# Kernel tuning notes

Hardware: AMD Instinct MI355X
Metric: run time of the kernel (lower is better)

The kernel has to match this reference:

```python
import jax, jax.numpy as jnp
import numpy as np

NH, HD = 12, 64          # heads, head dim (d_model=768)
SC = HD ** -0.5          # both Attention and CA_Attention use head_dim**-0.5


def patchify(x, p1, p2):
    # 'b c (h p1) (w p2) -> b (h w) (p1 p2 c)'
    B, C, H, W = x.shape
    h, w = H // p1, W // p2
    x = x.reshape(B, C, h, p1, w, p2).transpose(0, 2, 4, 3, 5, 1)  # b h w p1 p2 c
    return x.reshape(B, h * w, p1 * p2 * C)


def unpatchify(x, h, w, p1, p2, c):
    # 'b (h w) (p1 p2 c) -> b c (h p1) (w p2)'
    B = x.shape[0]
    x = x.reshape(B, h, w, p1, p2, c).transpose(0, 5, 1, 3, 2, 4)
    return x.reshape(B, c, h * p1, w * p2)


def ln(x, g, b):
    m = x.mean(-1, keepdims=True)
    v = ((x - m) ** 2).mean(-1, keepdims=True)
    return (x - m) / jnp.sqrt(v + 1e-5) * g + b


def setup_inputs() -> dict:
    key = jax.random.key(0)
    specs = [
        ('img_feats', (2, 32, 112, 112, 80)), ('txt', (2, 77, 768)),
        ('pe_w_ax', (1120, 768)), ('pe_b_ax', (768,)),
        ('pe_w_sag', (1120, 768)), ('pe_b_sag', (768,)),
        ('pe_w_cor', (1568, 768)), ('pe_b_cor', (768,)),
        ('pos_ax', (1, 256, 768)), ('pos_sag', (1, 256, 768)), ('pos_cor', (1, 256, 768)),
        ('qw', (768, 768)), ('kw', (768, 768)), ('vw', (768, 768)),
        ('pw', (768, 768)), ('pb', (768,)),
        ('caq_w', (768, 768)), ('caq_b', (768,)), ('cak_w', (768, 768)), ('cak_b', (768,)),
        ('cav_w', (768, 768)), ('cav_b', (768,)), ('cao_w', (768, 768)), ('cao_b', (768,)),
        ('mlp_w1', (768, 3072)), ('mlp_b1', (3072,)), ('mlp_w2', (3072, 768)), ('mlp_b2', (768,)),
        ('ow_ax', (768, 1120)), ('ob_ax', (1120,)),
        ('ow_sag', (768, 1120)), ('ob_sag', (1120,)),
        ('ow_cor', (768, 1568)), ('ob_cor', (1568,)),
    ]
    big = {'img_feats', 'txt', 'pos_ax', 'pos_sag', 'pos_cor'}
    out = {}
    for k, (n, s) in zip(jax.random.split(key, len(specs)), specs):
        scale = 1.0 if n in big else 0.02
        out[n] = jax.random.normal(k, s, jnp.float32) * scale
    out['view_w'] = jnp.ones((3,), jnp.float32)
    for n in ('n1_g', 'n2_g', 'n3_g'):
        out[n] = jnp.ones((768,), jnp.float32)
    for n in ('n1_b', 'n2_b', 'n3_b'):
        out[n] = jnp.zeros((768,), jnp.float32)
    return out


def reference(img_feats, txt, pe_w_ax, pe_b_ax, pe_w_sag, pe_b_sag, pe_w_cor, pe_b_cor,
              pos_ax, pos_sag, pos_cor, view_w, qw, kw, vw, pw, pb,
              caq_w, caq_b, cak_w, cak_b, cav_w, cav_b, cao_w, cao_b,
              n1_g, n1_b, n2_g, n2_b, n3_g, n3_b,
              mlp_w1, mlp_b1, mlp_w2, mlp_b2,
              ow_ax, ob_ax, ow_sag, ob_sag, ow_cor, ob_cor):

    def img_attn(t):
        B, N, C = t.shape
        q = (t @ qw).reshape(B, N, NH, HD)
        k = (t @ kw).reshape(B, N, NH, HD)
        v = (t @ vw).reshape(B, N, NH, HD)
        a = jax.nn.softmax(jnp.einsum('bnkc,bmkc->bknm', q, k) * SC, axis=-1)
        x = jnp.einsum('bknm,bmkc->bnkc', a, v).reshape(B, N, C)
        return x @ pw + pb

    def ca_attn(t, im):
        B, T, _ = t.shape
        N = im.shape[1]
        qh = (t @ caq_w + caq_b).reshape(B, T, NH, HD).transpose(0, 2, 1, 3)
        kh = (im @ cak_w + cak_b).reshape(B, N, NH, HD).transpose(0, 2, 1, 3)
        vh = (im @ cav_w + cav_b).reshape(B, N, NH, HD).transpose(0, 2, 1, 3)
        a = jax.nn.softmax(jnp.einsum('bhid,bhjd->bhij', qh, kh) * SC, axis=-1)
        # faithful to original einsum 'b h i j, b h j d -> b h j d' (sums over i)
        o = jnp.einsum('bhij,bhjd->bhjd', a, vh)
        o = o.transpose(0, 2, 1, 3).reshape(B, N, NH * HD)
        return o @ cao_w + cao_b

    def branch(v2d, pe_w, pe_b, pos, ow, ob, p1, p2):
        B, C, H, W = v2d.shape
        h, w = H // p1, W // p2
        q = patchify(v2d, p1, p2) @ pe_w + pe_b + pos
        q = ln(q, n1_g, n1_b)
        q = q + img_attn(q)
        q = ln(q, n2_g, n2_b)
        x = q + ca_attn(txt, q)
        x = x + (jax.nn.gelu(ln(x, n3_g, n3_b) @ mlp_w1 + mlp_b1, approximate=False) @ mlp_w2 + mlp_b2)
        return unpatchify(x @ ow + ob, h, w, p1, p2, C)

    # adaptive_avg_pool3d to size-1 along one axis == mean over that axis
    ax = img_feats.mean(2)    # (B,C,H,W)
    sag = img_feats.mean(3)   # (B,C,D,W)
    cor = img_feats.mean(4)   # (B,C,D,H)
    oax = branch(ax, pe_w_ax, pe_b_ax, pos_ax, ow_ax, ob_ax, 7, 5)
    osag = branch(sag, pe_w_sag, pe_b_sag, pos_sag, ow_sag, ob_sag, 7, 5)
    ocor = branch(cor, pe_w_cor, pe_b_cor, pos_cor, ow_cor, ob_cor, 7, 7)
    v3 = (view_w[0] * oax[:, :, None] + view_w[1] * osag[:, :, :, None]
          + view_w[2] * ocor[:, :, :, :, None])
    return img_feats + v3
```

## Files before the change

kernel.cpp:

```cpp
#include <hip/hip_runtime.h>
#include <math.h>

typedef __attribute__((ext_vector_type(8))) short s8;
typedef __attribute__((ext_vector_type(4))) float f4;
typedef unsigned short u16;

__device__ inline u16 f2bf(float f) {
    unsigned u = __float_as_uint(f);
    u += 0x7fffu + ((u >> 16) & 1u);
    return (u16)(u >> 16);
}
__device__ inline float bf2f(u16 x) {
    return __uint_as_float(((unsigned)x) << 16);
}
#define MFMA16(a, b, c) __builtin_amdgcn_mfma_f32_16x16x32_bf16(a, b, c, 0, 0, 0)

struct TT {
    const float* in[16];
    u16* out[16];
    int K[16];
    int N[16];
    int start[16];
    int total;
};

__global__ __launch_bounds__(256) void prep_k(TT tab, const float* __restrict__ img,
                                              float* __restrict__ axp,
                                              float* __restrict__ sag,
                                              float* __restrict__ cor) {
    __shared__ float sl[112*81];
    int bid = blockIdx.x;
    int t = threadIdx.x;
    if (bid < 1024) {
        int dc = bid & 15, bc = bid >> 4;
        int d0 = dc * 7;
        f4 axr[9];
        #pragma unroll
        for (int k = 0; k < 9; ++k) axr[k] = (f4){0.f,0.f,0.f,0.f};
        const float* base = img + (size_t)bc * 1003520 + (size_t)d0 * 8960;
        for (int sidx = 0; sidx < 7; ++sidx) {
            const f4* sp = reinterpret_cast<const f4*>(base + (size_t)sidx * 8960);
            #pragma unroll
            for (int k = 0; k < 9; ++k) {
                int q = t + k * 256;
                if (q < 2240) {
                    f4 v = __builtin_nontemporal_load(&sp[q]);
                    axr[k] += v;
                    int h = q / 20, w4 = q % 20;
                    float* row = &sl[h * 81 + w4 * 4];
                    row[0] = v[0]; row[1] = v[1]; row[2] = v[2]; row[3] = v[3];
                }
            }
            __syncthreads();
            if (t < 112) {
                float acc = 0.f;
                #pragma unroll 8
                for (int w = 0; w < 80; ++w) acc += sl[t * 81 + w];
                cor[((size_t)bc * 112 + d0 + sidx) * 112 + t] = acc * (1.f / 80.f);
            } else if (t < 192) {
                int w = t - 112;
                float acc = 0.f;
                #pragma unroll 8
                for (int h = 0; h < 112; ++h) acc += sl[h * 81 + w];
                sag[((size_t)bc * 112 + d0 + sidx) * 80 + w] = acc * (1.f / 112.f);
            }
            __syncthreads();
        }
        float* axo = axp + ((size_t)dc * 64 + bc) * 8960;
        #pragma unroll
        for (int k = 0; k < 9; ++k) {
            int q = t + k * 256;
            if (q < 2240) *reinterpret_cast<f4*>(axo + q * 4) = axr[k];
        }
        return;
    }
    int tb = bid - 1024;
    float (*tl)[33] = reinterpret_cast<float(*)[33]>(sl);
    int e = 0;
    #pragma unroll
    for (int i = 1; i < 16; ++i) if (tb >= tab.start[i]) e = i;
    const float* in = tab.in[e];
    u16* out = tab.out[e];
    int K = tab.K[e], N = tab.N[e];
    int tid = tb - tab.start[e];
    int nt = N >> 5;
    int k0 = (tid / nt) * 32, n0 = (tid % nt) * 32;
    int r = t >> 5, c = t & 31;
    #pragma unroll
    for (int i = 0; i < 4; ++i) tl[r + i*8][c] = in[(long)(k0 + r + i*8)*N + n0 + c];
    __syncthreads();
    #pragma unroll
    for (int i = 0; i < 4; ++i) out[(long)(n0 + r + i*8)*K + k0 + c] = f2bf(tl[c][r + i*8]);
}

__global__ __launch_bounds__(256) void patchify3_k(const float* __restrict__ axp,
                                                   const float* __restrict__ m_sag,
                                                   const float* __restrict__ m_cor,
                                                   u16* __restrict__ P0, u16* __restrict__ P1,
                                                   u16* __restrict__ P2) {
    __shared__ float sl[32][113];
    int br = blockIdx.y;
    int X = blockIdx.x;
    int b = X / 112, rem = X % 112;
    int hh = rem / 7, pp1 = rem % 7;
    const float* src; u16* dst; int Wt, p2, PD;
    if (br == 0)      { src = nullptr; dst = P0; Wt = 80;  p2 = 5; PD = 1120; }
    else if (br == 1) { src = m_sag;   dst = P1; Wt = 80;  p2 = 5; PD = 1120; }
    else              { src = m_cor;   dst = P2; Wt = 112; p2 = 7; PD = 1568; }
    int t = threadIdx.x;
    int row = hh*7 + pp1;
    int wq = Wt >> 2;
    if (br == 0) {
        for (int i = t; i < 32*20; i += 256) {
            int c = i / 20, w4 = i % 20;
            f4 s = (f4){0.f,0.f,0.f,0.f};
            size_t base = ((size_t)(b*32 + c)*112 + row)*80 + w4*4;
            #pragma unroll
            for (int p = 0; p < 16; ++p)
                s += *reinterpret_cast<const f4*>(axp + (size_t)p*573440 + base);
            s *= (1.f/112.f);
            sl[c][w4*4+0] = s[0]; sl[c][w4*4+1] = s[1]; sl[c][w4*4+2] = s[2]; sl[c][w4*4+3] = s[3];
        }
    } else {
        for (int i = t; i < 32*wq; i += 256) {
            int c = i / wq, w4 = i % wq;
            float4 v = *reinterpret_cast<const float4*>(
                src + ((size_t)(b*32 + c)*112 + row)*Wt + w4*4);
            sl[c][w4*4+0] = v.x; sl[c][w4*4+1] = v.y; sl[c][w4*4+2] = v.z; sl[c][w4*4+3] = v.w;
        }
    }
    __syncthreads();
    int tot = 16 * p2 * 32;
    for (int o = t; o < tot; o += 256) {
        int ww = o / (p2*32), rest = o % (p2*32);
        int pp2 = rest >> 5, c = rest & 31;
        dst[((size_t)(b*256 + hh*16 + ww))*PD + (pp1*p2 + pp2)*32 + c]
            = f2bf(sl[c][ww*p2 + pp2]);
    }
}

__device__ inline void load_tile(const u16* __restrict__ P, int ld, int nrows, int K,
                                 int r0, int k0, int t, s8 v[4]) {
    #pragma unroll
    for (int i = 0; i < 4; ++i) {
        int chunk = t + i*256;
        int row = chunk >> 4, c8 = (chunk & 15) * 8;
        s8 x;
        #pragma unroll
        for (int q = 0; q < 8; ++q) x[q] = 0;
        if (r0 + row < nrows && k0 + c8 < K)
            x = *reinterpret_cast<const s8*>(P + (long)(r0 + row)*ld + k0 + c8);
        v[i] = x;
    }
}
__device__ inline void load_tile_f32(const float* __restrict__ P, int ld, int nrows, int K,
                                     int r0, int k0, int t, s8 v[4]) {
    #pragma unroll
    for (int i = 0; i < 4; ++i) {
        int chunk = t + i*256;
        int row = chunk >> 4, c8 = (chunk & 15) * 8;
        s8 x;
        #pragma unroll
        for (int q = 0; q < 8; ++q) x[q] = 0;
        if (r0 + row < nrows && k0 + c8 < K) {
            const float* src = P + (long)(r0 + row)*ld + k0 + c8;
            #pragma unroll
            for (int q = 0; q < 8; ++q) x[q] = (short)f2bf(src[q]);
        }
        v[i] = x;
    }
}
__device__ inline void write_tile(u16 (*S)[136], int t, const s8 v[4]) {
    #pragma unroll
    for (int i = 0; i < 4; ++i) {
        int chunk = t + i*256;
        *reinterpret_cast<s8*>(&S[chunk >> 4][(chunk & 15)*8]) = v[i];
    }
}
__device__ inline void mfma_tile(const u16 (*As)[136], const u16 (*Bs)[136],
                                 int wr, int wc, int lane, f4 acc[2][2]) {
    int lrow = lane & 15;
    #pragma unroll
    for (int kh = 0; kh < 4; ++kh) {
        int lk = kh*32 + (lane >> 4) * 8;
        s8 af0 = *reinterpret_cast<const s8*>(&As[wr*32 + lrow][lk]);
        s8 af1 = *reinterpret_cast<const s8*>(&As[wr*32 + 16 + lrow][lk]);
        s8 bg0 = *reinterpret_cast<const s8*>(&Bs[wc*32 + lrow][lk]);
        s8 bg1 = *reinterpret_cast<const s8*>(&Bs[wc*32 + 16 + lrow][lk]);
        acc[0][0] = MFMA16(af0, bg0, acc[0][0]);
        acc[0][1] = MFMA16(af0, bg1, acc[0][1]);
        acc[1][0] = MFMA16(af1, bg0, acc[1][0]);
        acc[1][1] = MFMA16(af1, bg1, acc[1][1]);
    }
}

__global__ __launch_bounds__(256) void gemm_bf(
    const u16* __restrict__ A, const u16* __restrict__ Bt,
    float* __restrict__ Cf, u16* __restrict__ Cb,
    int M, int N, int K,
    const float* __restrict__ bias, const float* __restrict__ bias2,
    const float* __restrict__ resid, int act, u16* __restrict__ vt)
{
    __shared__ u16 As[2][64][136];
    __shared__ u16 Bs[2][64][136];
    int t = threadIdx.x;
    int m0 = blockIdx.y * 64, n0 = blockIdx.x * 64;
    int wave = t >> 6, lane = t & 63;
    int wr = wave >> 1, wc = wave & 1;
    f4 acc[2][2];
    #pragma unroll
    for (int m = 0; m < 2; ++m)
        #pragma unroll
        for (int n = 0; n < 2; ++n)
            #pragma unroll
            for (int r = 0; r < 4; ++r) acc[m][n][r] = 0.f;
    int nk = (K + 127) >> 7;
    s8 pa[4], pbv[4];
    load_tile(A, K, M, K, m0, 0, t, pa);
    load_tile(Bt, K, N, K, n0, 0, t, pbv);
    write_tile(As[0], t, pa);
    write_tile(Bs[0], t, pbv);
    __syncthreads();
    for (int kt = 0; kt < nk; ++kt) {
        int cur = kt & 1;
        if (kt + 1 < nk) {
            load_tile(A, K, M, K, m0, (kt+1) << 7, t, pa);
            load_tile(Bt, K, N, K, n0, (kt+1) << 7, t, pbv);
        }
        mfma_tile(As[cur], Bs[cur], wr, wc, lane, acc);
        if (kt + 1 < nk) {
            write_tile(As[cur^1], t, pa);
            write_tile(Bs[cur^1], t, pbv);
        }
        __syncthreads();
    }
    #pragma unroll
    for (int m = 0; m < 2; ++m) {
        int rbase = m0 + wr*32 + m*16 + (lane >> 4) * 4;
        #pragma unroll
        for (int n = 0; n < 2; ++n) {
            int col = n0 + wc*32 + n*16 + (lane & 15);
            if (col >= N) continue;
            #pragma unroll
            for (int r = 0; r < 4; ++r) {
                int row = rbase + r;
                if (row >= M) continue;
                float v = acc[m][n][r];
                if (bias) {
                    float bb = bias2 ? ((col < 768) ? bias[col] : bias2[col - 768]) : bias[col];
                    v += bb;
                }
                if (resid) v += resid[(long)row * N + col];
                if (act == 1) v = 0.5f * v * (1.0f + erff(v * 0.70710678118654752f));
                long ci = (long)row * N + col;
                u16 b = f2bf(v);
                if (Cf) Cf[ci] = v;
                if (Cb) Cb[ci] = b;
                if (vt && col >= 1536) {
                    int z = (row >> 8) * 12 + ((col - 1536) >> 6);
                    vt[((long)z * 64 + (col & 63)) * 256 + (row & 255)] = b;
                }
            }
        }
    }
}

struct PeDesc {
    const u16* A[3];
    const u16* Bt[4];
    const float* bias[4];
    const float* pos[3];
    int K[4];
    int M[4];
};

__global__ __launch_bounds__(256) void gemm_pe(PeDesc d, const float* __restrict__ txtf,
                                               float* __restrict__ C, u16* __restrict__ QHb) {
    int z = blockIdx.z;
    int M = d.M[z], K = d.K[z];
    int m0 = blockIdx.y * 64, n0 = blockIdx.x * 64;
    if (m0 >= M) return;
    __shared__ u16 As[2][64][136];
    __shared__ u16 Bs[2][64][136];
    const u16* Bb = d.Bt[z];
    const float* bias = d.bias[z];
    int t = threadIdx.x;
    int wave = t >> 6, lane = t & 63;
    int wr = wave >> 1, wc = wave & 1;
    f4 acc[2][2];
    #pragma unroll
    for (int m = 0; m < 2; ++m)
        #pragma unroll
        for (int n = 0; n < 2; ++n)
            #pragma unroll
            for (int r = 0; r < 4; ++r) acc[m][n][r] = 0.f;
    int nk = (K + 127) >> 7;
    s8 pa[4], pbv[4];
    if (z < 3) load_tile(d.A[z], K, M, K, m0, 0, t, pa);
    else       load_tile_f32(txtf, K, M, K, m0, 0, t, pa);
    load_tile(Bb, K, 768, K, n0, 0, t, pbv);
    write_tile(As[0], t, pa);
    write_tile(Bs[0], t, pbv);
    __syncthreads();
    for (int kt = 0; kt < nk; ++kt) {
        int cur = kt & 1;
        if (kt + 1 < nk) {
            if (z < 3) load_tile(d.A[z], K, M, K, m0, (kt+1) << 7, t, pa);
            else       load_tile_f32(txtf, K, M, K, m0, (kt+1) << 7, t, pa);
            load_tile(Bb, K, 768, K, n0, (kt+1) << 7, t, pbv);
        }
        mfma_tile(As[cur], Bs[cur], wr, wc, lane, acc);
        if (kt + 1 < nk) {
            write_tile(As[cur^1], t, pa);
            write_tile(Bs[cur^1], t, pbv);
        }
        __syncthreads();
    }
    #pragma unroll
    for (int m = 0; m < 2; ++m) {
        int rbase = m0 + wr*32 + m*16 + (lane >> 4) * 4;
        #pragma unroll
        for (int n = 0; n < 2; ++n) {
            int col = n0 + wc*32 + n*16 + (lane & 15);
            #pragma unroll
            for (int r = 0; r < 4; ++r) {
                int row = rbase + r;
                if (row >= M) continue;
                float v = acc[m][n][r] + bias[col];
                if (z < 3) {
                    v += d.pos[z][(long)(row & 255)*768 + col];
                    C[((long)z*512 + row) * 768 + col] = v;
                } else {
                    QHb[(long)row * 768 + col] = f2bf(v);
                }
            }
        }
    }
}

struct OwDesc {
    const u16* Bt[3];
    float* plane[3];
    const float* bias[3];
    int N[3];
    int p2[3];
    int Wd[3];
};

__global__ __launch_bounds__(256) void gemm_ow(OwDesc d, const u16* __restrict__ A,
                                               const float* __restrict__ vwp) {
    int z = blockIdx.z;
    int N = d.N[z];
    int n0 = blockIdx.x * 64;
    if (n0 >= N) return;
    __shared__ u16 As[2][64][136];
    __shared__ u16 Bs[2][64][136];
    const u16* Ab = A + (long)z * 512 * 768;
    const u16* Bb = d.Bt[z];
    int t = threadIdx.x;
    int m0 = blockIdx.y * 64;
    int wave = t >> 6, lane = t & 63;
    int wr = wave >> 1, wc = wave & 1;
    f4 acc[2][2];
    #pragma unroll
    for (int m = 0; m < 2; ++m)
        #pragma unroll
        for (int n = 0; n < 2; ++n)
            #pragma unroll
            for (int r = 0; r < 4; ++r) acc[m][n][r] = 0.f;
    s8 pa[4], pbv[4];
    load_tile(Ab, 768, 512, 768, m0, 0, t, pa);
    load_tile(Bb, 768, N, 768, n0, 0, t, pbv);
    write_tile(As[0], t, pa);
    write_tile(Bs[0], t, pbv);
    __syncthreads();
    for (int kt = 0; kt < 6; ++kt) {
        int cur = kt & 1;
        if (kt + 1 < 6) {
            load_tile(Ab, 768, 512, 768, m0, (kt+1) << 7, t, pa);
            load_tile(Bb, 768, N, 768, n0, (kt+1) << 7, t, pbv);
        }
        mfma_tile(As[cur], Bs[cur], wr, wc, lane, acc);
        if (kt + 1 < 6) {
            write_tile(As[cur^1], t, pa);
            write_tile(Bs[cur^1], t, pbv);
        }
        __syncthreads();
    }
    float* plane = d.plane[z];
    const float* bias = d.bias[z];
    int p2 = d.p2[z], Wd = d.Wd[z];
    float wt = vwp[z];
    #pragma unroll
    for (int m = 0; m < 2; ++m) {
        int rbase = m0 + wr*32 + m*16 + (lane >> 4) * 4;
        #pragma unroll
        for (int n = 0; n < 2; ++n) {
            int col = n0 + wc*32 + n*16 + (lane & 15);
            if (col >= N) continue;
            int pp = col >> 5, c = col & 31;
            int pp1 = pp / p2, pp2 = pp % p2;
            float bv = bias[col];
            #pragma unroll
            for (int r = 0; r < 4; ++r) {
                int row = rbase + r;
                int b = row >> 8, nn = row & 255;
                int hh = nn >> 4, ww = nn & 15;
                plane[((long)(b*32 + c)*112 + hh*7 + pp1)*Wd + ww*p2 + pp2]
                    = wt * (acc[m][n][r] + bv);
            }
        }
    }
}

__global__ __launch_bounds__(256) void ln_k(const float* __restrict__ in,
                                            float* __restrict__ outf,
                                            u16* __restrict__ outb,
                                            const float* __restrict__ g,
                                            const float* __restrict__ bta) {
    constexpr int N = 768;
    int row = blockIdx.x;
    const float* x = in + (size_t)row * N;
    int t = threadIdx.x;
    float v0 = x[t], v1 = x[t+256], v2 = x[t+512];
    float s = v0+v1+v2, s2 = v0*v0+v1*v1+v2*v2;
    #pragma unroll
    for (int off = 32; off > 0; off >>= 1) { s += __shfl_down(s, off); s2 += __shfl_down(s2, off); }
    __shared__ float red[8];
    int wid = t >> 6, lane = t & 63;
    if (lane == 0) { red[wid] = s; red[wid+4] = s2; }
    __syncthreads();
    if (t == 0) {
        float S = red[0]+red[1]+red[2]+red[3];
        float S2 = red[4]+red[5]+red[6]+red[7];
        float mean = S * (1.f/N);
        float var = S2 * (1.f/N) - mean*mean;
        red[0] = mean; red[1] = rsqrtf(var + 1e-5f);
    }
    __syncthreads();
    float mean = red[0], rstd = red[1];
    float y0 = (v0-mean)*rstd*g[t]     + bta[t];
    float y1 = (v1-mean)*rstd*g[t+256] + bta[t+256];
    float y2 = (v2-mean)*rstd*g[t+512] + bta[t+512];
    if (outf) {
        float* y = outf + (size_t)row * N;
        y[t] = y0; y[t+256] = y1; y[t+512] = y2;
    }
    if (outb) {
        u16* y = outb + (size_t)row * N;
        y[t] = f2bf(y0); y[t+256] = f2bf(y1); y[t+512] = f2bf(y2);
    }
}

__global__ __launch_bounds__(256) void attn_k(const u16* __restrict__ QKV,
                                              const u16* __restrict__ Vt,
                                              u16* __restrict__ O) {
    __shared__ u16 Ks[256][72];
    __shared__ u16 Ps[128][264];
    __shared__ u16 Vs[64][264];
    int zz = blockIdx.x;
    int bh = zz >> 1, half = zz & 1;
    int bb = bh / 12, h = bh % 12;
    long qrow0 = (long)bb*256 + half*128;
    int hcol = h*64;
    int t = threadIdx.x;
    int wave = t >> 6, lane = t & 63;
    int lr = lane & 15, lg = lane >> 4;
    #pragma unroll
    for (int i = 0; i < 8; ++i) {
        int chunk = t + i*256;
        int row = chunk >> 3, c8 = (chunk & 7)*8;
        *reinterpret_cast<s8*>(&Ks[row][c8]) =
            *reinterpret_cast<const s8*>(QKV + ((long)bb*256 + row)*2304 + 768 + hcol + c8);
    }
    #pragma unroll
    for (int i = 0; i < 8; ++i) {
        int chunk = t + i*256;
        int d = chunk >> 5, j8 = (chunk & 31)*8;
        *reinterpret_cast<s8*>(&Vs[d][j8]) =
            *reinterpret_cast<const s8*>(Vt + (long)bh*16384 + (long)d*256 + j8);
    }
    __syncthreads();
    f4 acc[2][16];
    #pragma unroll
    for (int m = 0; m < 2; ++m)
        #pragma unroll
        for (int n = 0; n < 16; ++n)
            #pragma unroll
            for (int r = 0; r < 4; ++r) acc[m][n][r] = 0.f;
    #pragma unroll
    for (int kh = 0; kh < 2; ++kh) {
        s8 af0 = *reinterpret_cast<const s8*>(QKV + (qrow0 + wave*32 + lr)*2304 + hcol + kh*32 + lg*8);
        s8 af1 = *reinterpret_cast<const s8*>(QKV + (qrow0 + wave*32 + 16 + lr)*2304 + hcol + kh*32 + lg*8);
        #pragma unroll
        for (int n = 0; n < 16; ++n) {
            s8 bf = *reinterpret_cast<const s8*>(&Ks[n*16 + lr][kh*32 + lg*8]);
            acc[0][n] = MFMA16(af0, bf, acc[0][n]);
            acc[1][n] = MFMA16(af1, bf, acc[1][n]);
        }
    }
    #pragma unroll
    for (int m = 0; m < 2; ++m)
        #pragma unroll
        for (int r = 0; r < 4; ++r) {
            float mx = -1e30f;
            #pragma unroll
            for (int n = 0; n < 16; ++n) mx = fmaxf(mx, acc[m][n][r]);
            #pragma unroll
            for (int o = 8; o; o >>= 1) mx = fmaxf(mx, __shfl_xor(mx, o));
            float l = 0.f;
            float p[16];
            #pragma unroll
            for (int n = 0; n < 16; ++n) {
                p[n] = __expf((acc[m][n][r] - mx) * 0.125f);
                l += p[n];
            }
            #pragma unroll
            for (int o = 8; o; o >>= 1) l += __shfl_xor(l, o);
            float inv = 1.f / l;
            int prow = wave*32 + m*16 + lg*4 + r;
            #pragma unroll
            for (int n = 0; n < 16; ++n)
                Ps[prow][n*16 + lr] = f2bf(p[n] * inv);
        }
    __syncthreads();
    f4 o2[2][4];
    #pragma unroll
    for (int m = 0; m < 2; ++m)
        #pragma unroll
        for (int n = 0; n < 4; ++n)
            #pragma unroll
            for (int r = 0; r < 4; ++r) o2[m][n][r] = 0.f;
    #pragma unroll
    for (int kh = 0; kh < 8; ++kh) {
        s8 pf0 = *reinterpret_cast<const s8*>(&Ps[wave*32 + lr][kh*32 + lg*8]);
        s8 pf1 = *reinterpret_cast<const s8*>(&Ps[wave*32 + 16 + lr][kh*32 + lg*8]);
        #pragma unroll
        for (int n = 0; n < 4; ++n) {
            s8 vf = *reinterpret_cast<const s8*>(&Vs[n*16 + lr][kh*32 + lg*8]);
            o2[0][n] = MFMA16(pf0, vf, o2[0][n]);
            o2[1][n] = MFMA16(pf1, vf, o2[1][n]);
        }
    }
    #pragma unroll
    for (int m = 0; m < 2; ++m)
        #pragma unroll
        for (int n = 0; n < 4; ++n)
            #pragma unroll
            for (int r = 0; r < 4; ++r)
                O[(qrow0 + wave*32 + m*16 + lg*4 + r)*768 + hcol + n*16 + lr] = f2bf(o2[m][n][r]);
}

__global__ __launch_bounds__(256) void ca_fused(const u16* __restrict__ QHb,
                                                const u16* __restrict__ KVHb,
                                                u16* __restrict__ O) {
    __shared__ u16 QHs[80][72];
    __shared__ u16 KHs[256][72];
    __shared__ float rmax[80][4];
    __shared__ float rsum[80][4];
    __shared__ float Wj[256];
    int bh = blockIdx.x;
    int rowblk = bh / 12, h = bh % 12;
    int bsel = rowblk & 1;
    int t = threadIdx.x;
    int wave = t >> 6, lane = t & 63;
    int lr = lane & 15, lg = lane >> 4;
    #pragma unroll
    for (int i = 0; i < 3; ++i) {
        int chunk = t + i*256;
        if (chunk < 640) {
            int row = chunk >> 3, c8 = (chunk & 7)*8;
            s8 v;
            #pragma unroll
            for (int q = 0; q < 8; ++q) v[q] = 0;
            if (row < 77)
                v = *reinterpret_cast<const s8*>(QHb + ((long)(bsel*77 + row))*768 + h*64 + c8);
            *reinterpret_cast<s8*>(&QHs[row][c8]) = v;
        }
    }
    #pragma unroll
    for (int i = 0; i < 8; ++i) {
        int chunk = t + i*256;
        int row = chunk >> 3, c8 = (chunk & 7)*8;
        *reinterpret_cast<s8*>(&KHs[row][c8]) =
            *reinterpret_cast<const s8*>(KVHb + ((long)rowblk*256 + row)*1536 + h*64 + c8);
    }
    __syncthreads();
    f4 acc[5][4];
    #pragma unroll
    for (int m = 0; m < 5; ++m)
        #pragma unroll
        for (int n = 0; n < 4; ++n)
            #pragma unroll
            for (int r = 0; r < 4; ++r) acc[m][n][r] = 0.f;
    #pragma unroll
    for (int kh = 0; kh < 2; ++kh) {
        s8 af[5], bf[4];
        #pragma unroll
        for (int m = 0; m < 5; ++m)
            af[m] = *reinterpret_cast<const s8*>(&QHs[m*16 + lr][kh*32 + lg*8]);
        #pragma unroll
        for (int n = 0; n < 4; ++n)
            bf[n] = *reinterpret_cast<const s8*>(&KHs[wave*64 + n*16 + lr][kh*32 + lg*8]);
        #pragma unroll
        for (int m = 0; m < 5; ++m)
            #pragma unroll
            for (int n = 0; n < 4; ++n)
                acc[m][n] = MFMA16(af[m], bf[n], acc[m][n]);
    }
    #pragma unroll
    for (int m = 0; m < 5; ++m)
        #pragma unroll
        for (int r = 0; r < 4; ++r) {
            float mx = -1e30f;
            #pragma unroll
            for (int n = 0; n < 4; ++n) mx = fmaxf(mx, acc[m][n][r]);
            #pragma unroll
            for (int o = 8; o; o >>= 1) mx = fmaxf(mx, __shfl_xor(mx, o));
            if (lr == 0) rmax[m*16 + lg*4 + r][wave] = mx;
        }
    __syncthreads();
    #pragma unroll
    for (int m = 0; m < 5; ++m)
        #pragma unroll
        for (int r = 0; r < 4; ++r) {
            int i = m*16 + lg*4 + r;
            float mi = fmaxf(fmaxf(rmax[i][0], rmax[i][1]), fmaxf(rmax[i][2], rmax[i][3]));
            float s = 0.f;
            #pragma unroll
            for (int n = 0; n < 4; ++n) s += __expf((acc[m][n][r] - mi) * 0.125f);
            #pragma unroll
            for (int o = 8; o; o >>= 1) s += __shfl_xor(s, o);
            if (lr == 0) rsum[i][wave] = s;
        }
    __syncthreads();
    float wn[4] = {0.f, 0.f, 0.f, 0.f};
    #pragma unroll
    for (int m = 0; m < 5; ++m)
        #pragma unroll
        for (int r = 0; r < 4; ++r) {
            int i = m*16 + lg*4 + r;
            if (i < 77) {
                float mi = fmaxf(fmaxf(rmax[i][0], rmax[i][1]), fmaxf(rmax[i][2], rmax[i][3]));
                float li = rsum[i][0] + rsum[i][1] + rsum[i][2] + rsum[i][3];
                float inv = 1.f / li;
                #pragma unroll
                for (int n = 0; n < 4; ++n)
                    wn[n] += __expf((acc[m][n][r] - mi) * 0.125f) * inv;
            }
        }
    #pragma unroll
    for (int n = 0; n < 4; ++n) {
        wn[n] += __shfl_xor(wn[n], 16);
        wn[n] += __shfl_xor(wn[n], 32);
    }
    if (lane < 16) {
        #pragma unroll
        for (int n = 0; n < 4; ++n) Wj[wave*64 + n*16 + lr] = wn[n];
    }
    __syncthreads();
    int d = t & 63;
    #pragma unroll 4
    for (int it = 0; it < 64; ++it) {
        int j = it*4 + (t >> 6);
        long row = (long)rowblk*256 + j;
        float vh = bf2f(KVHb[row*1536 + 768 + h*64 + d]);
        O[row*768 + h*64 + d] = f2bf(Wj[j] * vh);
    }
}

__global__ __launch_bounds__(256) void final_k(const float* __restrict__ img,
                                               const float* __restrict__ Aax,
                                               const float* __restrict__ Asag,
                                               const float* __restrict__ Acor,
                                               float* __restrict__ out) {
    int blk = blockIdx.x;
    int bc = blk / 112;
    const f4* ip = reinterpret_cast<const f4*>(img + (size_t)blk * 8960);
    const f4* ap = reinterpret_cast<const f4*>(Aax + (size_t)bc * 8960);
    const f4* sp = reinterpret_cast<const f4*>(Asag + (size_t)blk * 80);
    const float* cp = Acor + (size_t)blk * 112;
    f4* op = reinterpret_cast<f4*>(out + (size_t)blk * 8960);
    int t = threadIdx.x;
    #pragma unroll
    for (int k = 0; k < 9; ++k) {
        int q = t + k * 256;
        if (q < 2240) {
            f4 iv = __builtin_nontemporal_load(&ip[q]);
            int h = q / 20, w4 = q % 20;
            float cv = cp[h];
            f4 r = iv + ap[q] + sp[w4] + (f4){cv, cv, cv, cv};
            __builtin_nontemporal_store(r, &op[q]);
        }
    }
}

extern "C" void kernel_launch(void* const* d_in, const int* in_sizes, int n_in,
                              void* d_out, int out_size, void* d_ws, size_t ws_size,
                              hipStream_t stream) {
    (void)in_sizes; (void)n_in; (void)out_size; (void)ws_size;
    const float* img    = (const float*)d_in[0];
    const float* txt    = (const float*)d_in[1];
    const float* pe_w[3] = {(const float*)d_in[2], (const float*)d_in[4], (const float*)d_in[6]};
    const float* pe_b[3] = {(const float*)d_in[3], (const float*)d_in[5], (const float*)d_in[7]};
    const float* pos[3]  = {(const float*)d_in[8], (const float*)d_in[9], (const float*)d_in[10]};
    const float* qw = (const float*)d_in[11];
    const float* kw = (const float*)d_in[12];
    const float* vw_attn = (const float*)d_in[13];
    const float* pw = (const float*)d_in[14];
    const float* pb = (const float*)d_in[15];
    const float* caq_w = (const float*)d_in[16];
    const float* caq_b = (const float*)d_in[17];
    const float* cak_w = (const float*)d_in[18];
    const float* cak_b = (const float*)d_in[19];
    const float* cav_w = (const float*)d_in[20];
    const float* cav_b = (const float*)d_in[21];
    const float* cao_w = (const float*)d_in[22];
    const float* cao_b = (const float*)d_in[23];
    const float* mlp_w1 = (const float*)d_in[24];
    const float* mlp_b1 = (const float*)d_in[25];
    const float* mlp_w2 = (const float*)d_in[26];
    const float* mlp_b2 = (const float*)d_in[27];
    const float* ow[3] = {(const float*)d_in[28], (const float*)d_in[30], (const float*)d_in[32]};
    const float* ob[3] = {(const float*)d_in[29], (const float*)d_in[31], (const float*)d_in[33]};
    const float* view_w = (const float*)d_in[34];
    const float* n_g[3] = {(const float*)d_in[35], (const float*)d_in[36], (const float*)d_in[37]};
    const float* n_b[3] = {(const float*)d_in[38], (const float*)d_in[39], (const float*)d_in[40]};

    typedef unsigned short u16t;
    unsigned char* sb = (unsigned char*)d_out;
    size_t off = 0;
    auto B = [&](size_t bytes) -> void* {
        void* p = sb + off; off += (bytes + 511) & ~(size_t)511; return p;
    };
    u16t* qkvT  = (u16t*)B((size_t)2304*768*2);
    u16t* pwT   = (u16t*)B(768*768*2);
    u16t* caqT  = (u16t*)B(768*768*2);
    u16t* cakvT = (u16t*)B((size_t)1536*768*2);
    u16t* caoT  = (u16t*)B(768*768*2);
    u16t* mlp1T = (u16t*)B((size_t)3072*768*2);
    u16t* mlp2T = (u16t*)B((size_t)768*3072*2);
    u16t* peT[3]; peT[0] = (u16t*)B((size_t)768*1120*2); peT[1] = (u16t*)B((size_t)768*1120*2); peT[2] = (u16t*)B((size_t)768*1568*2);
    u16t* owT[3]; owT[0] = (u16t*)B((size_t)1120*768*2); owT[1] = (u16t*)B((size_t)1120*768*2); owT[2] = (u16t*)B((size_t)1568*768*2);
    float* axp   = (float*)B((size_t)16*573440*4);
    float* m_sag = (float*)B(573440*4);
    float* m_cor = (float*)B(802816*4);
    u16t* P0 = (u16t*)B((size_t)512*1120*2);
    u16t* P1 = (u16t*)B((size_t)512*1120*2);
    u16t* P2 = (u16t*)B((size_t)512*1568*2);
    float* X0  = (float*)B((size_t)1536*768*4);
    float* X1f = (float*)B((size_t)1536*768*4);
    float* X2  = (float*)B((size_t)1536*768*4);
    float* X3f = (float*)B((size_t)1536*768*4);
    float* X4  = (float*)B((size_t)1536*768*4);
    u16t* X1b = (u16t*)B((size_t)1536*768*2);
    u16t* X3b = (u16t*)B((size_t)1536*768*2);
    u16t* X5b = (u16t*)B((size_t)1536*768*2);
    u16t* X6b = (u16t*)B((size_t)1536*768*2);
    u16t* QKVb = (u16t*)B((size_t)1536*2304*2);
    u16t* Obf = (u16t*)B((size_t)1536*768*2);
    u16t* Vt  = (u16t*)B((size_t)72*64*256*2);
    u16t* Hb  = (u16t*)B((size_t)1536*3072*2);
    u16t* KVHb = (u16t*)B((size_t)1536*1536*2);
    u16t* QHb  = (u16t*)B((size_t)154*768*2);

    float* ws = (float*)d_ws;
    float* Aax  = ws;
    float* Asag = ws + 573440;
    float* Acor = ws + 1146880;

    TT tab;
    {
        const float* ins[16] = {qw, kw, vw_attn, pw, caq_w, cak_w, cav_w, cao_w,
                                mlp_w1, mlp_w2, pe_w[0], pe_w[1], pe_w[2], ow[0], ow[1], ow[2]};
        u16t* outs[16] = {qkvT, qkvT + 768*768, qkvT + 2*768*768, pwT, caqT, cakvT,
                          cakvT + 768*768, caoT, mlp1T, mlp2T, peT[0], peT[1], peT[2],
                          owT[0], owT[1], owT[2]};
        int Ks[16] = {768,768,768,768,768,768,768,768, 768,3072, 1120,1120,1568, 768,768,768};
        int Ns[16] = {768,768,768,768,768,768,768,768, 3072,768, 768,768,768, 1120,1120,1568};
        int st = 0;
        for (int i = 0; i < 16; ++i) {
            tab.in[i] = ins[i]; tab.out[i] = outs[i]; tab.K[i] = Ks[i]; tab.N[i] = Ns[i];
            tab.start[i] = st;
            st += (Ks[i] >> 5) * (Ns[i] >> 5);
        }
        tab.total = st;
        prep_k<<<1024 + st, 256, 0, stream>>>(tab, img, axp, m_sag, m_cor);
    }

    patchify3_k<<<dim3(224,3), 256, 0, stream>>>(axp, m_sag, m_cor, P0, P1, P2);

    auto gemm = [&](const u16t* A, const u16t* Bt, float* Cf, u16t* Cb,
                    int M, int N, int K, const float* bias, const float* bias2,
                    const float* resid, int act, u16t* vt) {
        dim3 g((N+63)/64, (M+63)/64, 1);
        gemm_bf<<<g, 256, 0, stream>>>(A, Bt, Cf, Cb, M, N, K, bias, bias2, resid, act, vt);
    };

    {
        PeDesc d;
        d.A[0] = P0; d.A[1] = P1; d.A[2] = P2;
        d.Bt[0] = peT[0]; d.Bt[1] = peT[1]; d.Bt[2] = peT[2]; d.Bt[3] = caqT;
        d.bias[0] = pe_b[0]; d.bias[1] = pe_b[1]; d.bias[2] = pe_b[2]; d.bias[3] = caq_b;
        d.pos[0] = pos[0]; d.pos[1] = pos[1]; d.pos[2] = pos[2];
        d.K[0] = 1120; d.K[1] = 1120; d.K[2] = 1568; d.K[3] = 768;
        d.M[0] = 512; d.M[1] = 512; d.M[2] = 512; d.M[3] = 154;
        gemm_pe<<<dim3(12,8,4), 256, 0, stream>>>(d, txt, X0, QHb);
    }

    ln_k<<<1536, 256, 0, stream>>>(X0, X1f, X1b, n_g[0], n_b[0]);
    gemm(X1b, qkvT, nullptr, QKVb, 1536, 2304, 768, nullptr, nullptr, nullptr, 0, Vt);
    attn_k<<<144, 256, 0, stream>>>(QKVb, Vt, Obf);
    gemm(Obf, pwT, X2, nullptr, 1536, 768, 768, pb, nullptr, X1f, 0, nullptr);
    ln_k<<<1536, 256, 0, stream>>>(X2, X3f, X3b, n_g[1], n_b[1]);
    gemm(X3b, cakvT, nullptr, KVHb, 1536, 1536, 768, cak_b, cav_b, nullptr, 0, nullptr);
    ca_fused<<<72, 256, 0, stream>>>(QHb, KVHb, Obf);
    gemm(Obf, caoT, X4, nullptr, 1536, 768, 768, cao_b, nullptr, X3f, 0, nullptr);
    ln_k<<<1536, 256, 0, stream>>>(X4, nullptr, X5b, n_g[2], n_b[2]);
    gemm(X5b, mlp1T, nullptr, Hb, 1536, 3072, 768, mlp_b1, nullptr, nullptr, 1, nullptr);
    gemm(Hb, mlp2T, nullptr, X6b, 1536, 768, 3072, mlp_b2, nullptr, X4, 0, nullptr);
    {
        OwDesc d;
        d.Bt[0] = owT[0]; d.Bt[1] = owT[1]; d.Bt[2] = owT[2];
        d.plane[0] = Aax; d.plane[1] = Asag; d.plane[2] = Acor;
        d.bias[0] = ob[0]; d.bias[1] = ob[1]; d.bias[2] = ob[2];
        d.N[0] = 1120; d.N[1] = 1120; d.N[2] = 1568;
        d.p2[0] = 5; d.p2[1] = 5; d.p2[2] = 7;
        d.Wd[0] = 80; d.Wd[1] = 80; d.Wd[2] = 112;
        gemm_ow<<<dim3(25,8,3), 256, 0, stream>>>(d, X6b, view_w);
    }

    final_k<<<7168, 256, 0, stream>>>(img, Aax, Asag, Acor, (float*)d_out);
}
```

Measured before the change: 416.2 us.

## Stage GEMM tiles with direct global-to-LDS loads and XOR swizzle

Rewrites the generic bf16 GEMM to stage A and B tiles with global_load_lds, writing straight into LDS instead of going through registers. Bank conflicts are avoided with an XOR-swizzled layout in place of the padded rows. Bounds checks are dropped and the grid now assumes M, N divisible by 64 and K divisible by 128. Register pressure and VGPR round-trips during prefetch should drop, but partial tiles are no longer supported.

Measured after the change: 405.7 us. 2.5% less time.

```diff
diff --git a/kernel.cpp b/kernel.cpp
--- a/kernel.cpp
+++ b/kernel.cpp
@@ -194,15 +194,15 @@
     }
 }
 
-__global__ __launch_bounds__(256) void gemm_bf(
+__global__ __launch_bounds__(256) void gemm_gl(
     const u16* __restrict__ A, const u16* __restrict__ Bt,
     float* __restrict__ Cf, u16* __restrict__ Cb,
     int M, int N, int K,
     const float* __restrict__ bias, const float* __restrict__ bias2,
     const float* __restrict__ resid, int act, u16* __restrict__ vt)
 {
-    __shared__ u16 As[2][64][136];
-    __shared__ u16 Bs[2][64][136];
+    __shared__ u16 As[2][64*128];
+    __shared__ u16 Bs[2][64*128];
     int t = threadIdx.x;
     int m0 = blockIdx.y * 64, n0 = blockIdx.x * 64;
     int wave = t >> 6, lane = t & 63;
@@ -214,37 +214,53 @@
         for (int n = 0; n < 2; ++n)
             #pragma unroll
             for (int r = 0; r < 4; ++r) acc[m][n][r] = 0.f;
-    int nk = (K + 127) >> 7;
-    s8 pa[4], pbv[4];
-    load_tile(A, K, M, K, m0, 0, t, pa);
-    load_tile(Bt, K, N, K, n0, 0, t, pbv);
-    write_tile(As[0], t, pa);
-    write_tile(Bs[0], t, pbv);
-    __syncthreads();
+    int nk = K >> 7;
+    auto stage = [&](int buf, int k0) {
+        #pragma unroll
+        for (int i = 0; i < 4; ++i) {
+            int c = wave*256 + i*64 + lane;
+            int row = c >> 4, jl = c & 15;
+            int jg = jl ^ (row & 7);
+            const u16* ga = A  + (long)(m0 + row)*K + k0 + jg*8;
+            const u16* gb = Bt + (long)(n0 + row)*K + k0 + jg*8;
+            u16* la = &As[buf][(wave*256 + i*64) * 8];
+            u16* lb = &Bs[buf][(wave*256 + i*64) * 8];
+            __builtin_amdgcn_global_load_lds((const unsigned int*)ga, (unsigned int*)la, 16, 0, 0);
+            __builtin_amdgcn_global_load_lds((const unsigned int*)gb, (unsigned int*)lb, 16, 0, 0);
+        }
+    };
+    stage(0, 0);
+    __syncthreads();
+    int lrow = lane & 15, lg = lane >> 4;
+    int r0a = wr*32 + lrow, r1a = r0a + 16;
+    int r0b = wc*32 + lrow, r1b = r0b + 16;
+    int sa = r0a & 7, sbx = r0b & 7;
     for (int kt = 0; kt < nk; ++kt) {
         int cur = kt & 1;
-        if (kt + 1 < nk) {
-            load_tile(A, K, M, K, m0, (kt+1) << 7, t, pa);
-            load_tile(Bt, K, N, K, n0, (kt+1) << 7, t, pbv);
-        }
-        mfma_tile(As[cur], Bs[cur], wr, wc, lane, acc);
-        if (kt + 1 < nk) {
-            write_tile(As[cur^1], t, pa);
-            write_tile(Bs[cur^1], t, pbv);
+        if (kt + 1 < nk) stage(cur ^ 1, (kt + 1) << 7);
+        #pragma unroll
+        for (int kh = 0; kh < 4; ++kh) {
+            int j = kh*4 + lg;
+            s8 af0 = *reinterpret_cast<const s8*>(&As[cur][r0a*128 + ((j ^ sa) << 3)]);
+            s8 af1 = *reinterpret_cast<const s8*>(&As[cur][r1a*128 + ((j ^ sa) << 3)]);
+            s8 bg0 = *reinterpret_cast<const s8*>(&Bs[cur][r0b*128 + ((j ^ sbx) << 3)]);
+            s8 bg1 = *reinterpret_cast<const s8*>(&Bs[cur][r1b*128 + ((j ^ sbx) << 3)]);
+            acc[0][0] = MFMA16(af0, bg0, acc[0][0]);
+            acc[0][1] = MFMA16(af0, bg1, acc[0][1]);
+            acc[1][0] = MFMA16(af1, bg0, acc[1][0]);
+            acc[1][1] = MFMA16(af1, bg1, acc[1][1]);
         }
         __syncthreads();
     }
     #pragma unroll
     for (int m = 0; m < 2; ++m) {
-        int rbase = m0 + wr*32 + m*16 + (lane >> 4) * 4;
+        int rbase = m0 + wr*32 + m*16 + lg*4;
         #pragma unroll
         for (int n = 0; n < 2; ++n) {
-            int col = n0 + wc*32 + n*16 + (lane & 15);
-            if (col >= N) continue;
+            int col = n0 + wc*32 + n*16 + lrow;
             #pragma unroll
             for (int r = 0; r < 4; ++r) {
                 int row = rbase + r;
-                if (row >= M) continue;
                 float v = acc[m][n][r];
                 if (bias) {
                     float bb = bias2 ? ((col < 768) ? bias[col] : bias2[col - 768]) : bias[col];
@@ -793,8 +809,8 @@
     auto gemm = [&](const u16t* A, const u16t* Bt, float* Cf, u16t* Cb,
                     int M, int N, int K, const float* bias, const float* bias2,
                     const float* resid, int act, u16t* vt) {
-        dim3 g((N+63)/64, (M+63)/64, 1);
-        gemm_bf<<<g, 256, 0, stream>>>(A, Bt, Cf, Cb, M, N, K, bias, bias2, resid, act, vt);
+        dim3 g(N/64, M/64, 1);
+        gemm_gl<<<g, 256, 0, stream>>>(A, Bt, Cf, Cb, M, N, K, bias, bias2, resid, act, vt);
     };
 
     {
```
